# Kernel tuning notes

Hardware: AMD Instinct MI355X
Metric: run time of the kernel (lower is better)

The kernel has to match this reference:

```python
import jax, jax.numpy as jnp
import numpy as np

N_EMBD = 1024
N_HEAD = 16
EPS = 1e-5


def _layernorm(x, g, b):
    mu = jnp.mean(x, axis=-1, keepdims=True)
    var = jnp.mean(jnp.square(x - mu), axis=-1, keepdims=True)
    return (x - mu) * jax.lax.rsqrt(var + EPS) * g + b


def setup_inputs() -> dict:
    key = jax.random.key(0)
    ks = jax.random.split(key, 8)
    e = N_EMBD
    s = 0.02
    return {
        "x": jax.random.normal(ks[0], (4, 2048, e), dtype=jnp.float32),
        "ln1_g": jnp.ones((e,), jnp.float32),
        "ln1_b": jnp.zeros((e,), jnp.float32),
        "w_attn": jax.random.normal(ks[1], (e, 3 * e), jnp.float32) * s,
        "b_attn": jnp.zeros((3 * e,), jnp.float32),
        "w_proj": jax.random.normal(ks[2], (e, e), jnp.float32) * s,
        "b_proj": jnp.zeros((e,), jnp.float32),
        "ln2_g": jnp.ones((e,), jnp.float32),
        "ln2_b": jnp.zeros((e,), jnp.float32),
        "w_fc": jax.random.normal(ks[3], (e, 4 * e), jnp.float32) * s,
        "b_fc": jnp.zeros((4 * e,), jnp.float32),
        "w_fc2": jax.random.normal(ks[4], (4 * e, e), jnp.float32) * s,
        "b_fc2": jnp.zeros((e,), jnp.float32),
    }


def reference(x, ln1_g, ln1_b, w_attn, b_attn, w_proj, b_proj,
              ln2_g, ln2_b, w_fc, b_fc, w_fc2, b_fc2):
    b, s, e = x.shape
    h = N_HEAD
    d = e // h

    # --- attention sublayer (pre-LN) ---
    xn = _layernorm(x, ln1_g, ln1_b)
    qkv = xn @ w_attn + b_attn                      # [b, s, 3e]
    qkv = qkv.reshape(b, s, 3, h, d)
    q = jnp.transpose(qkv[:, :, 0], (0, 2, 1, 3))   # [b, h, s, d]
    k = jnp.transpose(qkv[:, :, 1], (0, 2, 1, 3))
    v = jnp.transpose(qkv[:, :, 2], (0, 2, 1, 3))

    mask = jnp.triu(jnp.ones((s, s), x.dtype), k=1) * jnp.asarray(-1e10, x.dtype)
    attn = jnp.einsum('bhqd,bhkd->bhqk', q, k) / jnp.sqrt(jnp.asarray(d, x.dtype))
    attn = jax.nn.softmax(attn + mask, axis=-1)
    out = jnp.einsum('bhqk,bhkd->bhqd', attn, v)    # [b, h, s, d]
    out = jnp.transpose(out, (0, 2, 1, 3)).reshape(b, s, e)
    x = x + (out @ w_proj + b_proj)

    # --- MLP sublayer (pre-LN) ---
    xn = _layernorm(x, ln2_g, ln2_b)
    hdn = jax.nn.gelu(xn @ w_fc + b_fc, approximate=False)
    x = x + (hdn @ w_fc2 + b_fc2)
    return x
```

## Files before the change

### kernel.cpp

```cpp
#include <hip/hip_runtime.h>

typedef unsigned short u16;
typedef unsigned int u32;
typedef __attribute__((ext_vector_type(8))) short bf16x8;
typedef __attribute__((ext_vector_type(4))) float f32x4;
typedef __attribute__((ext_vector_type(4))) u32 u32x4;

#define DEV __device__ __forceinline__
#define MFMA16(a, b, c) __builtin_amdgcn_mfma_f32_16x16x32_bf16(a, b, c, 0, 0, 0)

DEV u16 f2bf(float f) {
  u32 u = __float_as_uint(f);
  u32 r = (u + 0x7fffu + ((u >> 16) & 1u)) >> 16;
  return (u16)r;
}

DEV void async16(const void* g, void* l) {
  __builtin_amdgcn_global_load_lds((const __attribute__((address_space(1))) u32*)g,
                                   (__attribute__((address_space(3))) u32*)l, 16, 0, 0);
}

__global__ __launch_bounds__(256)
void wt_transpose(const float* __restrict__ w, u16* __restrict__ wt, int K, int N) {
  __shared__ float tile[32][33];
  int n0 = blockIdx.x * 32;
  int k0 = blockIdx.y * 32;
  int tx = threadIdx.x;
  int ty = threadIdx.y;
#pragma unroll
  for (int i = 0; i < 4; ++i)
    tile[ty + 8 * i][tx] = w[(size_t)(k0 + ty + 8 * i) * N + n0 + tx];
  __syncthreads();
#pragma unroll
  for (int i = 0; i < 4; ++i) {
    int n = ty + 8 * i;
    wt[(size_t)(n0 + n) * K + k0 + tx] = f2bf(tile[tx][n]);
  }
}

__global__ __launch_bounds__(256)
void ln_kernel(const float* __restrict__ x, const float* __restrict__ g,
               const float* __restrict__ b, u16* __restrict__ out) {
  int row = blockIdx.x;
  int tid = threadIdx.x;
  const float4* xr = (const float4*)(x + (size_t)row * 1024);
  float4 v = xr[tid];
  float s = v.x + v.y + v.z + v.w;
  float ss = v.x * v.x + v.y * v.y + v.z * v.z + v.w * v.w;
#pragma unroll
  for (int o = 32; o > 0; o >>= 1) {
    s += __shfl_down(s, o);
    ss += __shfl_down(ss, o);
  }
  __shared__ float ps[4], pss[4];
  if ((tid & 63) == 0) { ps[tid >> 6] = s; pss[tid >> 6] = ss; }
  __syncthreads();
  s = ps[0] + ps[1] + ps[2] + ps[3];
  ss = pss[0] + pss[1] + pss[2] + pss[3];
  float mu = s * (1.0f / 1024.0f);
  float var = ss * (1.0f / 1024.0f) - mu * mu;
  float rs = rsqrtf(var + 1e-5f);
  float4 gg = ((const float4*)g)[tid];
  float4 bb = ((const float4*)b)[tid];
  ushort4 ov;
  ov.x = f2bf((v.x - mu) * rs * gg.x + bb.x);
  ov.y = f2bf((v.y - mu) * rs * gg.y + bb.y);
  ov.z = f2bf((v.z - mu) * rs * gg.z + bb.z);
  ov.w = f2bf((v.w - mu) * rs * gg.w + bb.w);
  *(ushort4*)(out + (size_t)row * 1024 + tid * 4) = ov;
}

__global__ __launch_bounds__(256)
void v_transpose(const u16* __restrict__ v, u16* __restrict__ vt) {
  __shared__ u16 t[64][72];
  int s0 = blockIdx.x * 64;
  int bh = blockIdx.y;
  int tid = threadIdx.x;
  const u16* src = v + ((size_t)bh * 2048 + s0) * 64;
#pragma unroll
  for (int p = 0; p < 2; ++p) {
    int r = p * 32 + (tid >> 3);
    int c = (tid & 7) * 8;
    u32x4 a = *(const u32x4*)(src + r * 64 + c);
    const u16* pa = (const u16*)&a;
#pragma unroll
    for (int j = 0; j < 8; ++j) t[r][c + j] = pa[j];
  }
  __syncthreads();
  u16* dst = vt + (size_t)bh * 131072 + s0;
#pragma unroll
  for (int p = 0; p < 2; ++p) {
    int d = p * 32 + (tid >> 3);
    int sc = (tid & 7) * 8;
    u32x4 a;
    u16* pa = (u16*)&a;
#pragma unroll
    for (int j = 0; j < 8; ++j) pa[j] = t[sc + j][d];
    *(u32x4*)(dst + (size_t)d * 2048 + sc) = a;
  }
}

DEV void stage128x32(const u16* __restrict__ src, long ld, long r0, char* lds, int tid) {
  int wid = tid >> 6;
  const char* g0 = (const char*)(src + r0 * ld);
#pragma unroll
  for (int i = 0; i < 2; ++i) {
    long row = i * 64 + (tid >> 2);
    long cg = tid & 3;
    async16(g0 + (row * ld + cg * 8) * 2, lds + i * 4096 + wid * 1024);
  }
}

template <int EPI>
__global__ __launch_bounds__(256, 2)
void gemm128(const u16* __restrict__ A, const u16* __restrict__ Bt,
             const float* __restrict__ bias, int M, int N, int K,
             float* __restrict__ outf, u16* __restrict__ outb,
             const float* __restrict__ res,
             u16* __restrict__ qp, u16* __restrict__ kp, u16* __restrict__ vp) {
  __shared__ char lds[16384];
  char* ldsA = lds;
  char* ldsB = lds + 8192;
  int tid = threadIdx.x;
  int lane = tid & 63, wid = tid >> 6;
  int wr = wid >> 1, wc = wid & 1;
  long m0 = (long)blockIdx.y * 128;
  long n0 = (long)blockIdx.x * 128;

  f32x4 acc[4][4];
#pragma unroll
  for (int i = 0; i < 4; ++i)
#pragma unroll
    for (int j = 0; j < 4; ++j) acc[i][j] = (f32x4)0.0f;

  int lrow = lane & 15;
  int lkb = (lane >> 4) * 16;

  for (int k0 = 0; k0 < K; k0 += 32) {
    stage128x32(A + k0, K, m0, ldsA, tid);
    stage128x32(Bt + k0, K, n0, ldsB, tid);
    __syncthreads();
    bf16x8 af[4], bfr[4];
#pragma unroll
    for (int mi = 0; mi < 4; ++mi)
      af[mi] = *(const bf16x8*)(ldsA + (wr * 64 + mi * 16 + lrow) * 64 + lkb);
#pragma unroll
    for (int ni = 0; ni < 4; ++ni)
      bfr[ni] = *(const bf16x8*)(ldsB + (wc * 64 + ni * 16 + lrow) * 64 + lkb);
#pragma unroll
    for (int mi = 0; mi < 4; ++mi)
#pragma unroll
      for (int ni = 0; ni < 4; ++ni)
        acc[mi][ni] = MFMA16(af[mi], bfr[ni], acc[mi][ni]);
    __syncthreads();
  }

  int rgrp = (lane >> 4) * 4;
#pragma unroll
  for (int mi = 0; mi < 4; ++mi) {
#pragma unroll
    for (int ni = 0; ni < 4; ++ni) {
      long col = n0 + wc * 64 + ni * 16 + (lane & 15);
      float bv = bias[col];
#pragma unroll
      for (int r = 0; r < 4; ++r) {
        long row = m0 + wr * 64 + mi * 16 + rgrp + r;
        float c = acc[mi][ni][r] + bv;
        if (EPI == 0) {
          int part = (int)(col >> 10);
          int hd = (int)(col & 1023);
          long bq = row >> 11;
          long sq = row & 2047;
          long dst = (((bq << 4) + (hd >> 6)) * 2048 + sq) * 64 + (hd & 63);
          if (part == 0) qp[dst] = f2bf(c * 0.125f);
          else if (part == 1) kp[dst] = f2bf(c);
          else vp[dst] = f2bf(c);
        } else if (EPI == 1) {
          long idx = row * (long)N + col;
          outf[idx] = c + res[idx];
        } else {
          float gl = 0.5f * c * (1.0f + erff(c * 0.70710678118f));
          outb[row * (long)N + col] = f2bf(gl);
        }
      }
    }
  }
}

__global__ __launch_bounds__(256, 2)
void attn_kernel(const u16* __restrict__ q, const u16* __restrict__ k,
                 const u16* __restrict__ vt, u16* __restrict__ outp) {
  __shared__ char ldsK[2][8192];
  __shared__ char ldsV[2][8192];
  __shared__ char ldsP[4][4096];
  int lin = blockIdx.x + 8 * blockIdx.y;
  int xcd = lin & 7, pos = lin >> 3;
  int j = pos >> 3;
  int bh = ((pos & 7) << 3) | xcd;
  int tid = threadIdx.x, lane = tid & 63, w = tid >> 6;
  const u16* qb = q + (size_t)bh * 131072;
  const u16* kb = k + (size_t)bh * 131072;
  const u16* vb = vt + (size_t)bh * 131072;

  int lr = lane & 15, lg = lane >> 4;
  int swz = (lr & 7) << 4;

  const int qih = 15 - j, qil = j;
  const int NTH = 2 * qih + 2;
  const int NTL = 2 * qil + 2;

  const bf16x8 ones = (bf16x8)(short)0x3F80;

  bf16x8 qf[2][2][2];
#pragma unroll
  for (int p = 0; p < 2; ++p) {
    int q0p = (p ? qil : qih) * 128;
#pragma unroll
    for (int fq = 0; fq < 2; ++fq) {
      const u16* qr = qb + (size_t)(q0p + w * 32 + fq * 16 + lr) * 64 + lg * 8;
      qf[p][fq][0] = *(const bf16x8*)(qr);
      qf[p][fq][1] = *(const bf16x8*)(qr + 32);
    }
  }

  f32x4 o[2][2][4];
  f32x4 lacc[2][2];
  float m_run[2][2][4];
#pragma unroll
  for (int p = 0; p < 2; ++p)
#pragma unroll
    for (int fq = 0; fq < 2; ++fq) {
      lacc[p][fq] = (f32x4)0.0f;
#pragma unroll
      for (int i = 0; i < 4; ++i) {
        o[p][fq][i] = (f32x4)0.0f;
        m_run[p][fq][i] = -1e30f;
      }
    }

  auto stage = [&](int buf, int t) {
    int kv0 = t * 64;
    const char* gk = (const char*)(kb + (size_t)kv0 * 64);
#pragma unroll
    for (int i = 0; i < 2; ++i) {
      int off = i * 4096 + tid * 16;
      int src = off ^ (((off >> 7) & 7) << 4);
      async16(gk + src, &ldsK[buf][i * 4096 + w * 1024]);
    }
#pragma unroll
    for (int i = 0; i < 2; ++i) {
      int vrow = i * 32 + (tid >> 3);
      int cb = ((tid & 7) * 16) ^ ((vrow & 7) << 4);
      async16((const char*)vb + (size_t)vrow * 4096 + (size_t)kv0 * 2 + cb,
              &ldsV[buf][i * 4096 + w * 1024]);
    }
  };

  stage(0, 0);
  __syncthreads();
  int cur = 0;

  for (int t = 0; t < NTH; ++t) {
    if (t + 1 < NTH) stage(cur ^ 1, t + 1);
    int kv0 = t * 64;

#pragma unroll
    for (int p = 0; p < 2; ++p) {
      if (p == 1 && t >= NTL) break;
      int q0p = (p ? qil : qih) * 128;
      int ntp = p ? NTL : NTH;

      f32x4 s[2][4];
      __builtin_amdgcn_s_setprio(1);
#pragma unroll
      for (int nf = 0; nf < 4; ++nf) {
#pragma unroll
        for (int fq = 0; fq < 2; ++fq) s[fq][nf] = (f32x4)0.0f;
#pragma unroll
        for (int ks = 0; ks < 2; ++ks) {
          bf16x8 kf = *(const bf16x8*)(&ldsK[cur][(nf * 16 + lr) * 128 +
                                                 ((ks * 64 + lg * 16) ^ swz)]);
#pragma unroll
          for (int fq = 0; fq < 2; ++fq)
            s[fq][nf] = MFMA16(qf[p][fq][ks], kf, s[fq][nf]);
        }
      }
      __builtin_amdgcn_s_setprio(0);

      if (t + 2 >= ntp) {
#pragma unroll
        for (int fq = 0; fq < 2; ++fq)
#pragma unroll
          for (int nf = 0; nf < 4; ++nf)
#pragma unroll
            for (int r = 0; r < 4; ++r) {
              int qrow = q0p + w * 32 + fq * 16 + lg * 4 + r;
              int kvc = kv0 + nf * 16 + lr;
              if (kvc > qrow) s[fq][nf][r] = -1e30f;
            }
      }

      float pmx[2][4];
      bool need = false;
#pragma unroll
      for (int fq = 0; fq < 2; ++fq)
#pragma unroll
        for (int r = 0; r < 4; ++r) {
          pmx[fq][r] = fmaxf(fmaxf(s[fq][0][r], s[fq][1][r]),
                             fmaxf(s[fq][2][r], s[fq][3][r]));
          need = need || (pmx[fq][r] > m_run[p][fq][r] + 8.0f);
        }
      if (__any(need)) {
#pragma unroll
        for (int fq = 0; fq < 2; ++fq)
#pragma unroll
          for (int r = 0; r < 4; ++r) {
            float pm = pmx[fq][r];
#pragma unroll
            for (int m = 1; m < 16; m <<= 1) pm = fmaxf(pm, __shfl_xor(pm, m));
            float mnew = fmaxf(m_run[p][fq][r], pm);
            float al = __expf(m_run[p][fq][r] - mnew);
            m_run[p][fq][r] = mnew;
            lacc[p][fq][r] *= al;
#pragma unroll
            for (int nf = 0; nf < 4; ++nf) o[p][fq][nf][r] *= al;
          }
      }

#pragma unroll
      for (int fq = 0; fq < 2; ++fq)
#pragma unroll
        for (int nf = 0; nf < 4; ++nf)
#pragma unroll
          for (int r = 0; r < 4; ++r) {
            float pv = __expf(s[fq][nf][r] - m_run[p][fq][r]);
            int prow = fq * 16 + lg * 4 + r;
            int pb = ((nf * 16 + lr) * 2) ^ ((prow & 7) << 4);
            *(u16*)(&ldsP[w][prow * 128 + pb]) = (u16)(__float_as_uint(pv) >> 16);
          }

      __builtin_amdgcn_s_setprio(1);
#pragma unroll
      for (int ks = 0; ks < 2; ++ks) {
        bf16x8 pf[2];
#pragma unroll
        for (int fq = 0; fq < 2; ++fq)
          pf[fq] = *(const bf16x8*)(&ldsP[w][(fq * 16 + lr) * 128 +
                                             ((ks * 64 + lg * 16) ^ swz)]);
        lacc[p][0] = MFMA16(pf[0], ones, lacc[p][0]);
        lacc[p][1] = MFMA16(pf[1], ones, lacc[p][1]);
#pragma unroll
        for (int nf = 0; nf < 4; ++nf) {
          bf16x8 vf = *(const bf16x8*)(&ldsV[cur][(nf * 16 + lr) * 128 +
                                                 ((ks * 64 + lg * 16) ^ swz)]);
#pragma unroll
          for (int fq = 0; fq < 2; ++fq)
            o[p][fq][nf] = MFMA16(pf[fq], vf, o[p][fq][nf]);
        }
      }
      __builtin_amdgcn_s_setprio(0);
    }

    __syncthreads();
    cur ^= 1;
  }

  int b = bh >> 4, h = bh & 15;
#pragma unroll
  for (int p = 0; p < 2; ++p) {
    int q0p = (p ? qil : qih) * 128;
#pragma unroll
    for (int fq = 0; fq < 2; ++fq)
#pragma unroll
      for (int r = 0; r < 4; ++r) {
        int qrow = q0p + w * 32 + fq * 16 + lg * 4 + r;
        float inv = 1.0f / lacc[p][fq][r];
        size_t base = ((size_t)(b * 2048 + qrow)) * 1024 + h * 64;
#pragma unroll
        for (int nf = 0; nf < 4; ++nf)
          outp[base + nf * 16 + lr] = f2bf(o[p][fq][nf][r] * inv);
      }
  }
}

extern "C" void kernel_launch(void* const* d_in, const int* in_sizes, int n_in,
                              void* d_out, int out_size, void* d_ws, size_t ws_size,
                              hipStream_t stream) {
  const float* x      = (const float*)d_in[0];
  const float* ln1_g  = (const float*)d_in[1];
  const float* ln1_b  = (const float*)d_in[2];
  const float* w_attn = (const float*)d_in[3];
  const float* b_attn = (const float*)d_in[4];
  const float* w_proj = (const float*)d_in[5];
  const float* b_proj = (const float*)d_in[6];
  const float* ln2_g  = (const float*)d_in[7];
  const float* ln2_b  = (const float*)d_in[8];
  const float* w_fc   = (const float*)d_in[9];
  const float* b_fc   = (const float*)d_in[10];
  const float* w_fc2  = (const float*)d_in[11];
  const float* b_fc2  = (const float*)d_in[12];
  float* out = (float*)d_out;

  char* ws = (char*)d_ws;
  u16* wt_attn = (u16*)(ws + 0);
  u16* wt_proj = (u16*)(ws + 6291456);
  u16* wt_fc   = (u16*)(ws + 8388608);
  u16* wt_fc2  = (u16*)(ws + 16777216);
  u16* xn      = (u16*)(ws + 25165824);
  float* x2    = (float*)(ws + 41943040);
  char* region = ws + 75497472;
  u16* qb = (u16*)(region);
  u16* kb = (u16*)(region + 16777216);
  u16* vb = (u16*)(region + 33554432);
  u16* vt = (u16*)(region + 50331648);
  u16* ao = (u16*)(region + 67108864);
  u16* hm = (u16*)(region);

  dim3 tb(32, 8);
  wt_transpose<<<dim3(3072 / 32, 1024 / 32), tb, 0, stream>>>(w_attn, wt_attn, 1024, 3072);
  wt_transpose<<<dim3(1024 / 32, 1024 / 32), tb, 0, stream>>>(w_proj, wt_proj, 1024, 1024);
  wt_transpose<<<dim3(4096 / 32, 1024 / 32), tb, 0, stream>>>(w_fc, wt_fc, 1024, 4096);
  wt_transpose<<<dim3(1024 / 32, 4096 / 32), tb, 0, stream>>>(w_fc2, wt_fc2, 4096, 1024);

  ln_kernel<<<8192, 256, 0, stream>>>(x, ln1_g, ln1_b, xn);

  gemm128<0><<<dim3(3072 / 128, 8192 / 128), 256, 0, stream>>>(
      xn, wt_attn, b_attn, 8192, 3072, 1024,
      nullptr, nullptr, nullptr, qb, kb, vb);

  v_transpose<<<dim3(32, 64), 256, 0, stream>>>(vb, vt);

  attn_kernel<<<dim3(8, 64), 256, 0, stream>>>(qb, kb, vt, ao);

  gemm128<1><<<dim3(1024 / 128, 8192 / 128), 256, 0, stream>>>(
      ao, wt_proj, b_proj, 8192, 1024, 1024,
      x2, nullptr, x, nullptr, nullptr, nullptr);

  ln_kernel<<<8192, 256, 0, stream>>>(x2, ln2_g, ln2_b, xn);

  gemm128<2><<<dim3(4096 / 128, 8192 / 128), 256, 0, stream>>>(
      xn, wt_fc, b_fc, 8192, 4096, 1024,
      nullptr, hm, nullptr, nullptr, nullptr, nullptr);

  gemm128<1><<<dim3(1024 / 128, 8192 / 128), 256, 0, stream>>>(
      hm, wt_fc2, b_fc2, 8192, 1024, 4096,
      out, nullptr, x2, nullptr, nullptr, nullptr);
}
```

Measured before the change: 410.8 us.

## Widen GEMM K-tile to 64 with swizzled LDS and XCD-aware block remap

The bf16 GEMM now stages 128x64 tiles of A and B per iteration instead of 128x32, halving the number of barrier-separated K steps. LDS addresses are XOR-swizzled by row to avoid bank conflicts on the fragment reads. Blocks are remapped so that consecutive blocks on the same XCD share M rows for better L2 reuse, and MFMA sections are bracketed with s_setprio. The remap hardcodes eight row-blocks per XCD, so it assumes a grid height of 64. Doubling the LDS footprint to 32 KB may reduce occupancy headroom.

New measurement: 371.3 us. -9.6%, faster.

```diff
diff --git a/kernel.cpp b/kernel.cpp
--- a/kernel.cpp
+++ b/kernel.cpp
@@ -100,17 +100,6 @@
   }
 }
 
-DEV void stage128x32(const u16* __restrict__ src, long ld, long r0, char* lds, int tid) {
-  int wid = tid >> 6;
-  const char* g0 = (const char*)(src + r0 * ld);
-#pragma unroll
-  for (int i = 0; i < 2; ++i) {
-    long row = i * 64 + (tid >> 2);
-    long cg = tid & 3;
-    async16(g0 + (row * ld + cg * 8) * 2, lds + i * 4096 + wid * 1024);
-  }
-}
-
 template <int EPI>
 __global__ __launch_bounds__(256, 2)
 void gemm128(const u16* __restrict__ A, const u16* __restrict__ Bt,
@@ -118,49 +107,77 @@
              float* __restrict__ outf, u16* __restrict__ outb,
              const float* __restrict__ res,
              u16* __restrict__ qp, u16* __restrict__ kp, u16* __restrict__ vp) {
-  __shared__ char lds[16384];
-  char* ldsA = lds;
-  char* ldsB = lds + 8192;
-  int tid = threadIdx.x;
-  int lane = tid & 63, wid = tid >> 6;
-  int wr = wid >> 1, wc = wid & 1;
-  long m0 = (long)blockIdx.y * 128;
-  long n0 = (long)blockIdx.x * 128;
+  __shared__ char lds[32768];
+  const int tid = threadIdx.x;
+  const int lane = tid & 63, wid = tid >> 6;
+  const int wr = wid >> 1, wc = wid & 1;
+  const int lr = lane & 15, hi = lane >> 4;
+  const int swz = (lr & 7) << 4;
+
+  const int nbx = gridDim.x;
+  int lin = blockIdx.x + nbx * blockIdx.y;
+  int xcd = lin & 7, j = lin >> 3;
+  int bx = j % nbx;
+  int by = xcd * 8 + j / nbx;
+
+  const long m0 = (long)by * 128;
+  const long n0 = (long)bx * 128;
+  const long ldb = (long)K * 2;
+  const char* Abase = (const char*)A + m0 * ldb;
+  const char* Bbase = (const char*)Bt + n0 * ldb;
 
   f32x4 acc[4][4];
 #pragma unroll
   for (int i = 0; i < 4; ++i)
 #pragma unroll
-    for (int j = 0; j < 4; ++j) acc[i][j] = (f32x4)0.0f;
-
-  int lrow = lane & 15;
-  int lkb = (lane >> 4) * 16;
-
-  for (int k0 = 0; k0 < K; k0 += 32) {
-    stage128x32(A + k0, K, m0, ldsA, tid);
-    stage128x32(Bt + k0, K, n0, ldsB, tid);
+    for (int jj = 0; jj < 4; ++jj) acc[i][jj] = (f32x4)0.0f;
+
+  auto stage = [&](const char* base, int kt, int dst) {
+#pragma unroll
+    for (int l = 0; l < 4; ++l) {
+      int c = (wid * 4 + l) * 64 + lane;
+      int r = c >> 3, ch = c & 7;
+      async16(base + (long)kt * 128 + (long)r * ldb + ((ch * 16) ^ ((r & 7) << 4)),
+              lds + dst + (wid * 4 + l) * 1024);
+    }
+  };
+  auto rdA = [&](int mi, int kk) {
+    int rr = wr * 64 + mi * 16 + lr;
+    return *(const bf16x8*)(lds + rr * 128 + ((kk * 64 + hi * 16) ^ swz));
+  };
+  auto rdB = [&](int ni, int kk) {
+    int rr = wc * 64 + ni * 16 + lr;
+    return *(const bf16x8*)(lds + 16384 + rr * 128 + ((kk * 64 + hi * 16) ^ swz));
+  };
+
+  const int NT = K >> 6;
+  for (int kt = 0; kt < NT; ++kt) {
+    stage(Abase, kt, 0);
+    stage(Bbase, kt, 16384);
     __syncthreads();
-    bf16x8 af[4], bfr[4];
-#pragma unroll
-    for (int mi = 0; mi < 4; ++mi)
-      af[mi] = *(const bf16x8*)(ldsA + (wr * 64 + mi * 16 + lrow) * 64 + lkb);
-#pragma unroll
-    for (int ni = 0; ni < 4; ++ni)
-      bfr[ni] = *(const bf16x8*)(ldsB + (wc * 64 + ni * 16 + lrow) * 64 + lkb);
-#pragma unroll
-    for (int mi = 0; mi < 4; ++mi)
-#pragma unroll
-      for (int ni = 0; ni < 4; ++ni)
-        acc[mi][ni] = MFMA16(af[mi], bfr[ni], acc[mi][ni]);
+    bf16x8 a[4][2], b[4][2];
+#pragma unroll
+    for (int mi = 0; mi < 4; ++mi) { a[mi][0] = rdA(mi, 0); a[mi][1] = rdA(mi, 1); }
+#pragma unroll
+    for (int ni = 0; ni < 4; ++ni) { b[ni][0] = rdB(ni, 0); b[ni][1] = rdB(ni, 1); }
+    __builtin_amdgcn_s_setprio(1);
+#pragma unroll
+    for (int kk = 0; kk < 2; ++kk)
+#pragma unroll
+      for (int mi = 0; mi < 4; ++mi)
+#pragma unroll
+        for (int ni = 0; ni < 4; ++ni)
+          acc[mi][ni] = MFMA16(a[mi][kk], b[ni][kk], acc[mi][ni]);
+    __builtin_amdgcn_s_setprio(0);
     __syncthreads();
   }
 
-  int rgrp = (lane >> 4) * 4;
+  int rgrp = hi * 4;
 #pragma unroll
   for (int mi = 0; mi < 4; ++mi) {
 #pragma unroll
     for (int ni = 0; ni < 4; ++ni) {
-      long col = n0 + wc * 64 + ni * 16 + (lane & 15);
+      long col = n0 + wc * 64 + ni * 16 + lr;
       float bv = bias[col];
 #pragma unroll
       for (int r = 0; r < 4; ++r) {
```
